# Kernel tuning notes

Hardware: AMD Instinct MI355X
Metric: run time of the kernel (lower is better)

The kernel has to match this reference:

```python
import jax, jax.numpy as jnp
import numpy as np

B, S, D, H = 256, 128, 2, 512


def _lstm_cell(x, h, c, Wih, Whh, bih, bhh):
    # PyTorch LSTMCell gate order: i, f, g, o
    z = x @ Wih.T + bih + h @ Whh.T + bhh
    i, f, g, o = jnp.split(z, 4, axis=-1)
    c_new = jax.nn.sigmoid(f) * c + jax.nn.sigmoid(i) * jnp.tanh(g)
    h_new = jax.nn.sigmoid(o) * jnp.tanh(c_new)
    return h_new, c_new


def setup_inputs() -> dict:
    key = jax.random.key(0)
    ks = jax.random.split(key, 16)
    sc = 0.05
    inp = {
        "x": jax.random.uniform(ks[0], (B, S, D), dtype=jnp.float32),
        "enc_Wih": jax.random.normal(ks[1], (4 * H, D), dtype=jnp.float32) * sc,
        "enc_Whh": jax.random.normal(ks[2], (4 * H, H), dtype=jnp.float32) * sc,
        "enc_bih": jax.random.normal(ks[3], (4 * H,), dtype=jnp.float32) * sc,
        "enc_bhh": jax.random.normal(ks[4], (4 * H,), dtype=jnp.float32) * sc,
        "dec_Wih": jax.random.normal(ks[5], (4 * H, H), dtype=jnp.float32) * sc,
        "dec_Whh": jax.random.normal(ks[6], (4 * H, H), dtype=jnp.float32) * sc,
        "dec_bih": jax.random.normal(ks[7], (4 * H,), dtype=jnp.float32) * sc,
        "dec_bhh": jax.random.normal(ks[8], (4 * H,), dtype=jnp.float32) * sc,
        "W1": jax.random.normal(ks[9], (H, H), dtype=jnp.float32) * sc,
        "b1": jax.random.normal(ks[10], (H,), dtype=jnp.float32) * sc,
        "W2": jax.random.normal(ks[11], (H, H), dtype=jnp.float32) * sc,
        "b2": jax.random.normal(ks[12], (H,), dtype=jnp.float32) * sc,
        "v": jax.random.normal(ks[13], (1, H), dtype=jnp.float32) * sc,
        "bv": jax.random.normal(ks[14], (1,), dtype=jnp.float32) * sc,
    }
    return inp


def reference(x, enc_Wih, enc_Whh, enc_bih, enc_bhh,
              dec_Wih, dec_Whh, dec_bih, dec_bhh,
              W1, b1, W2, b2, v, bv):
    # ---- encoder: LSTMCell scan over sequence ----
    def enc_step(carry, xt):
        h, c = carry
        h, c = _lstm_cell(xt, h, c, enc_Wih, enc_Whh, enc_bih, enc_bhh)
        return (h, c), h

    h0 = jnp.zeros((B, H), dtype=x.dtype)
    c0 = jnp.zeros((B, H), dtype=x.dtype)
    (h_enc, c_enc), enc_hs = jax.lax.scan(enc_step, (h0, c0),
                                          jnp.transpose(x, (1, 0, 2)))
    enc_hs = jnp.transpose(enc_hs, (1, 0, 2))          # [B, S, H]
    W1e = enc_hs @ W1.T + b1                            # [B, S, H]

    # ---- decoder with per-step additive attention ----
    dec_in = jnp.full((B, H), -1.0, dtype=x.dtype)      # constant decoder input

    def dec_step(carry, _):
        h, c = carry
        h, c = _lstm_cell(dec_in, h, c, dec_Wih, dec_Whh, dec_bih, dec_bhh)
        W2h = h @ W2.T + b2                             # [B, H]
        u = jnp.tanh(W1e + W2h[:, None, :]) @ v[0] + bv[0]  # [B, S]
        a = jax.nn.softmax(u, axis=1)                   # [B, S]
        h_new = jnp.einsum('bs,bsh->bh', a, enc_hs)     # attention glimpse
        return (h_new, c), a

    _, attn = jax.lax.scan(dec_step, (h_enc, c_enc), None, length=S)
    return jnp.transpose(attn, (1, 0, 2))               # [B, S, S]
```

## Files before the change

### kernel.cpp

```cpp
#include <hip/hip_runtime.h>

#define B_ 256
#define S_ 128
#define D_ 2
#define H_ 512
#define G4 2048

__device__ __forceinline__ float sigm(float x){ return 1.f/(1.f+__expf(-x)); }
__device__ __forceinline__ float tanh_(float x){ return 1.f - 2.f/(__expf(2.f*x)+1.f); }

__global__ __launch_bounds__(256) void prep_kernel(
    const float* __restrict__ dWih, const float* __restrict__ dbih,
    const float* __restrict__ dbhh, const float* __restrict__ ebih,
    const float* __restrict__ ebhh, float* __restrict__ dxw,
    float* __restrict__ ebias)
{
    int j = blockIdx.x * 256 + threadIdx.x;
    const float* row = dWih + (size_t)j * H_;
    float s = 0.f;
    for (int k = 0; k < H_; k++) s += row[k];
    dxw[j]   = dbih[j] + dbhh[j] - s;
    ebias[j] = ebih[j] + ebhh[j];
}

template<bool ENC>
__global__ __launch_bounds__(256) void lstm_step(
    const float* __restrict__ h_in, int h_stride,
    const float* __restrict__ c_in,
    const float* __restrict__ Whh,
    const float* __restrict__ xbias,
    const float* __restrict__ Wih,
    const float* __restrict__ xt,
    float* __restrict__ h_out, int ho_stride,
    float* __restrict__ c_out)
{
    __shared__ float Hs[32][34];
    __shared__ float Ws[32][68];

    const int tid = threadIdx.x;
    const int tx  = tid & 15;
    const int ty  = tid >> 4;
    const int b0  = blockIdx.x * 32;
    const int kh0 = blockIdx.y * 16;

    float acc[4][2];
#pragma unroll
    for (int g = 0; g < 4; g++) { acc[g][0] = 0.f; acc[g][1] = 0.f; }

    const int lk = tid & 31;
    const int lr = tid >> 5;

    float hreg[4], wreg[8];
#pragma unroll
    for (int i = 0; i < 4; i++) {
        int bl = lr + i * 8;
        hreg[i] = h_in[(size_t)(b0 + bl) * h_stride + lk];
    }
#pragma unroll
    for (int i = 0; i < 8; i++) {
        int p = lr + i * 8; int g = p & 3, kh = p >> 2;
        wreg[i] = Whh[(size_t)(g * H_ + kh0 + kh) * H_ + lk];
    }

    for (int c = 0; c < 16; c++) {
        __syncthreads();
#pragma unroll
        for (int i = 0; i < 4; i++) Hs[lk][lr + i * 8] = hreg[i];
#pragma unroll
        for (int i = 0; i < 8; i++) { int p = lr + i * 8; Ws[lk][p] = wreg[i]; }
        __syncthreads();
        if (c + 1 < 16) {
            int k0 = (c + 1) * 32;
#pragma unroll
            for (int i = 0; i < 4; i++) {
                int bl = lr + i * 8;
                hreg[i] = h_in[(size_t)(b0 + bl) * h_stride + k0 + lk];
            }
#pragma unroll
            for (int i = 0; i < 8; i++) {
                int p = lr + i * 8; int g = p & 3, kh = p >> 2;
                wreg[i] = Whh[(size_t)(g * H_ + kh0 + kh) * H_ + k0 + lk];
            }
        }
#pragma unroll
        for (int k = 0; k < 32; k++) {
            float2 hv = *(const float2*)&Hs[k][2 * ty];
            float4 wv = *(const float4*)&Ws[k][4 * tx];
            acc[0][0] += wv.x * hv.x;  acc[0][1] += wv.x * hv.y;
            acc[1][0] += wv.y * hv.x;  acc[1][1] += wv.y * hv.y;
            acc[2][0] += wv.z * hv.x;  acc[2][1] += wv.z * hv.y;
            acc[3][0] += wv.w * hv.x;  acc[3][1] += wv.w * hv.y;
        }
    }

    const int khid = kh0 + tx;
#pragma unroll
    for (int bb = 0; bb < 2; bb++) {
        int b = b0 + 2 * ty + bb;
        float zi = acc[0][bb] + xbias[0 * H_ + khid];
        float zf = acc[1][bb] + xbias[1 * H_ + khid];
        float zg = acc[2][bb] + xbias[2 * H_ + khid];
        float zo = acc[3][bb] + xbias[3 * H_ + khid];
        if constexpr (ENC) {
            float x0 = xt[b * (S_ * D_) + 0];
            float x1 = xt[b * (S_ * D_) + 1];
            zi += x0 * Wih[(0 * H_ + khid) * D_ + 0] + x1 * Wih[(0 * H_ + khid) * D_ + 1];
            zf += x0 * Wih[(1 * H_ + khid) * D_ + 0] + x1 * Wih[(1 * H_ + khid) * D_ + 1];
            zg += x0 * Wih[(2 * H_ + khid) * D_ + 0] + x1 * Wih[(2 * H_ + khid) * D_ + 1];
            zo += x0 * Wih[(3 * H_ + khid) * D_ + 0] + x1 * Wih[(3 * H_ + khid) * D_ + 1];
        }
        float c_old = c_in[(size_t)b * H_ + khid];
        float ig = sigm(zi), fg = sigm(zf), og = sigm(zo);
        float gg = tanh_(zg);
        float cn = fg * c_old + ig * gg;
        float hn = og * tanh_(cn);
        c_out[(size_t)b * H_ + khid] = cn;
        h_out[(size_t)b * ho_stride + khid] = hn;
    }
}

template<int BM, int BN, int TM, int TN>
__global__ __launch_bounds__((BM/TM)*(BN/TN)) void gemm_bias(
    const float* __restrict__ A, const float* __restrict__ Bm,
    const float* __restrict__ bias, float* __restrict__ C,
    int M, int N, int K)
{
    constexpr int BK = 32;
    constexpr int TH = (BM / TM) * (BN / TN);
    constexpr int AL = BM * BK / TH;
    constexpr int BL = BN * BK / TH;
    constexpr int RP = TH / BK;
    __shared__ float As[BK][BM + 4];
    __shared__ float Bs[BK][BN + 4];
    const int tid = threadIdx.x;
    const int tn = tid % (BN / TN);
    const int tm = tid / (BN / TN);
    const int m0 = blockIdx.x * BM, n0 = blockIdx.y * BN;
    const int lk = tid % BK, lr = tid / BK;

    float acc[TM][TN];
#pragma unroll
    for (int i = 0; i < TM; i++)
#pragma unroll
        for (int j = 0; j < TN; j++) acc[i][j] = 0.f;

    float areg[AL], breg[BL];
#pragma unroll
    for (int i = 0; i < AL; i++) areg[i] = A[(size_t)(m0 + lr + i * RP) * K + lk];
#pragma unroll
    for (int i = 0; i < BL; i++) breg[i] = Bm[(size_t)(n0 + lr + i * RP) * K + lk];

    const int NC = K / BK;
    for (int c = 0; c < NC; c++) {
        __syncthreads();
#pragma unroll
        for (int i = 0; i < AL; i++) As[lk][lr + i * RP] = areg[i];
#pragma unroll
        for (int i = 0; i < BL; i++) Bs[lk][lr + i * RP] = breg[i];
        __syncthreads();
        if (c + 1 < NC) {
            int k0 = (c + 1) * BK;
#pragma unroll
            for (int i = 0; i < AL; i++) areg[i] = A[(size_t)(m0 + lr + i * RP) * K + k0 + lk];
#pragma unroll
            for (int i = 0; i < BL; i++) breg[i] = Bm[(size_t)(n0 + lr + i * RP) * K + k0 + lk];
        }
#pragma unroll
        for (int k = 0; k < BK; k++) {
            float av[TM], bvv[TN];
#pragma unroll
            for (int i = 0; i < TM; i++) av[i] = As[k][tm * TM + i];
#pragma unroll
            for (int j = 0; j < TN; j++) bvv[j] = Bs[k][tn * TN + j];
#pragma unroll
            for (int i = 0; i < TM; i++)
#pragma unroll
                for (int j = 0; j < TN; j++) acc[i][j] += av[i] * bvv[j];
        }
    }
#pragma unroll
    for (int i = 0; i < TM; i++) {
        int m = m0 + tm * TM + i;
#pragma unroll
        for (int j = 0; j < TN; j++) {
            int n = n0 + tn * TN + j;
            C[(size_t)m * N + n] = acc[i][j] + bias[n];
        }
    }
}

__global__ __launch_bounds__(512) void attn_step(
    const float* __restrict__ W1e, const float* __restrict__ enc_hs,
    const float* __restrict__ W2h, const float* __restrict__ vv,
    const float* __restrict__ bv, float* __restrict__ out,
    float* __restrict__ h_glim, int t)
{
    __shared__ float q[H_];
    __shared__ float vs[H_];
    __shared__ float u[S_];
    __shared__ float red[8];

    const int b = blockIdx.x;
    const int tid = threadIdx.x;
    const int lane = tid & 63, wave = tid >> 6;

    q[tid]  = W2h[(size_t)b * H_ + tid];
    vs[tid] = vv[tid];
    __syncthreads();

    const float* w1b = W1e + (size_t)b * S_ * H_;
#pragma unroll 2
    for (int si = 0; si < 16; si++) {
        int s = wave * 16 + si;
        const float* row = w1b + (size_t)s * H_ + lane * 8;
        float4 r0 = *(const float4*)(row);
        float4 r1 = *(const float4*)(row + 4);
        float4 q0 = *(const float4*)&q[lane * 8];
        float4 q1 = *(const float4*)&q[lane * 8 + 4];
        float4 v0 = *(const float4*)&vs[lane * 8];
        float4 v1 = *(const float4*)&vs[lane * 8 + 4];
        float sum = tanh_(r0.x + q0.x) * v0.x + tanh_(r0.y + q0.y) * v0.y
                  + tanh_(r0.z + q0.z) * v0.z + tanh_(r0.w + q0.w) * v0.w
                  + tanh_(r1.x + q1.x) * v1.x + tanh_(r1.y + q1.y) * v1.y
                  + tanh_(r1.z + q1.z) * v1.z + tanh_(r1.w + q1.w) * v1.w;
#pragma unroll
        for (int off = 32; off; off >>= 1) sum += __shfl_xor(sum, off);
        if (lane == 0) u[s] = sum + bv[0];
    }
    __syncthreads();

    float e = 0.f;
    if (tid < 128) {
        float m = u[tid];
#pragma unroll
        for (int off = 32; off; off >>= 1) m = fmaxf(m, __shfl_xor(m, off));
        if ((tid & 63) == 0) red[tid >> 6] = m;
    }
    __syncthreads();
    float mx = fmaxf(red[0], red[1]);
    if (tid < 128) {
        e = __expf(u[tid] - mx);
        float ss = e;
#pragma unroll
        for (int off = 32; off; off >>= 1) ss += __shfl_xor(ss, off);
        if ((tid & 63) == 0) red[4 + (tid >> 6)] = ss;
    }
    __syncthreads();
    float denom = red[4] + red[5];
    if (tid < 128) {
        float a = e / denom;
        u[tid] = a;
        out[(size_t)b * S_ * S_ + (size_t)t * S_ + tid] = a;
    }
    __syncthreads();

    const float* eb = enc_hs + (size_t)b * S_ * H_;
    float acc = 0.f;
#pragma unroll 4
    for (int s = 0; s < S_; s++) acc += u[s] * eb[(size_t)s * H_ + tid];
    h_glim[(size_t)b * H_ + tid] = acc;
}

extern "C" void kernel_launch(void* const* d_in, const int* in_sizes, int n_in,
                              void* d_out, int out_size, void* d_ws, size_t ws_size,
                              hipStream_t stream)
{
    const float* x    = (const float*)d_in[0];
    const float* eWih = (const float*)d_in[1];
    const float* eWhh = (const float*)d_in[2];
    const float* ebih = (const float*)d_in[3];
    const float* ebhh = (const float*)d_in[4];
    const float* dWih = (const float*)d_in[5];
    const float* dWhh = (const float*)d_in[6];
    const float* dbih = (const float*)d_in[7];
    const float* dbhh = (const float*)d_in[8];
    const float* W1   = (const float*)d_in[9];
    const float* b1   = (const float*)d_in[10];
    const float* W2   = (const float*)d_in[11];
    const float* b2   = (const float*)d_in[12];
    const float* vv   = (const float*)d_in[13];
    const float* bv   = (const float*)d_in[14];
    float* out = (float*)d_out;

    float* ws      = (float*)d_ws;
    float* enc_hs  = ws;
    float* W1e     = enc_hs + (size_t)B_ * S_ * H_;
    float* h0      = W1e    + (size_t)B_ * S_ * H_;
    float* c_cur   = h0     + (size_t)B_ * H_;
    float* h_dec   = c_cur  + (size_t)B_ * H_;
    float* h_glim  = h_dec  + (size_t)B_ * H_;
    float* W2h     = h_glim + (size_t)B_ * H_;
    float* dxw     = W2h    + (size_t)B_ * H_;
    float* ebias   = dxw    + G4;

    hipMemsetAsync(h0, 0, (size_t)B_ * H_ * sizeof(float), stream);
    hipMemsetAsync(c_cur, 0, (size_t)B_ * H_ * sizeof(float), stream);
    prep_kernel<<<8, 256, 0, stream>>>(dWih, dbih, dbhh, ebih, ebhh, dxw, ebias);

    dim3 lgrid(B_ / 32, H_ / 16);

    for (int t = 0; t < S_; t++) {
        const float* h_in = (t == 0) ? h0 : (enc_hs + (size_t)(t - 1) * H_);
        int h_stride = (t == 0) ? H_ : S_ * H_;
        lstm_step<true><<<lgrid, 256, 0, stream>>>(
            h_in, h_stride, c_cur, eWhh, ebias, eWih, x + t * D_,
            enc_hs + (size_t)t * H_, S_ * H_, c_cur);
    }

    gemm_bias<64, 64, 4, 4><<<dim3((B_ * S_) / 64, H_ / 64), 256, 0, stream>>>(
        enc_hs, W1, b1, W1e, B_ * S_, H_, H_);

    for (int t = 0; t < S_; t++) {
        const float* h_in = (t == 0) ? (enc_hs + (size_t)(S_ - 1) * H_) : h_glim;
        int h_stride = (t == 0) ? S_ * H_ : H_;
        lstm_step<false><<<lgrid, 256, 0, stream>>>(
            h_in, h_stride, c_cur, dWhh, dxw, nullptr, nullptr,
            h_dec, H_, c_cur);
        gemm_bias<16, 32, 1, 2><<<dim3(B_ / 16, H_ / 32), 256, 0, stream>>>(
            h_dec, W2, b2, W2h, B_, H_, H_);
        attn_step<<<B_, 512, 0, stream>>>(W1e, enc_hs, W2h, vv, bv, out, h_glim, t);
    }
}
```

Measured before the change: 10.52 ms.

## Replace per-step kernel launches with persistent encoder/decoder kernels using grid barriers

Fuses the 128 encoder step launches and the 384 decoder launches into two persistent kernels of 256 blocks that synchronise through an atomic grid barrier. Each thread keeps its slice of the recurrent weight matrix (and of W2) in registers for the whole sequence, and the cell state stays in registers, so weights are not reloaded every step and launch overhead disappears. The risks are a hang if all 256 blocks are not co-resident, since nothing checks occupancy, plus the cost of grid-wide barrier latency and high register pressure from the 64-float weight arrays.

```diff
diff --git a/kernel.cpp b/kernel.cpp
--- a/kernel.cpp
+++ b/kernel.cpp
@@ -4,10 +4,29 @@
 #define S_ 128
 #define D_ 2
 #define H_ 512
-#define G4 2048
+#define NB 256
+#define NT 512
 
 __device__ __forceinline__ float sigm(float x){ return 1.f/(1.f+__expf(-x)); }
 __device__ __forceinline__ float tanh_(float x){ return 1.f - 2.f/(__expf(2.f*x)+1.f); }
+
+__device__ __forceinline__ void grid_barrier(unsigned* bar) {
+    __syncthreads();
+    if (threadIdx.x == 0) {
+        __threadfence();
+        unsigned g = __hip_atomic_load(&bar[1], __ATOMIC_RELAXED, __HIP_MEMORY_SCOPE_AGENT);
+        unsigned a = __hip_atomic_fetch_add(&bar[0], 1u, __ATOMIC_ACQ_REL, __HIP_MEMORY_SCOPE_AGENT);
+        if (a == NB - 1u) {
+            __hip_atomic_store(&bar[0], 0u, __ATOMIC_RELAXED, __HIP_MEMORY_SCOPE_AGENT);
+            __hip_atomic_store(&bar[1], g + 1u, __ATOMIC_RELEASE, __HIP_MEMORY_SCOPE_AGENT);
+        } else {
+            while (__hip_atomic_load(&bar[1], __ATOMIC_RELAXED, __HIP_MEMORY_SCOPE_AGENT) == g)
+                __builtin_amdgcn_s_sleep(2);
+            __threadfence();
+        }
+    }
+    __syncthreads();
+}
 
 __global__ __launch_bounds__(256) void prep_kernel(
     const float* __restrict__ dWih, const float* __restrict__ dbih,
@@ -23,99 +42,102 @@
     ebias[j] = ebih[j] + ebhh[j];
 }
 
-template<bool ENC>
-__global__ __launch_bounds__(256) void lstm_step(
-    const float* __restrict__ h_in, int h_stride,
-    const float* __restrict__ c_in,
-    const float* __restrict__ Whh,
-    const float* __restrict__ xbias,
-    const float* __restrict__ Wih,
-    const float* __restrict__ xt,
-    float* __restrict__ h_out, int ho_stride,
-    float* __restrict__ c_out)
+__global__ __launch_bounds__(NT, 2) void enc_kernel(
+    const float* __restrict__ x, const float* __restrict__ eWih,
+    const float* __restrict__ eWhh, const float* __restrict__ ebias,
+    float* enc_hs, float* c_fin, unsigned* bar)
 {
-    __shared__ float Hs[32][34];
-    __shared__ float Ws[32][68];
+    extern __shared__ float smem[];
+    float (*Hs)[H_]    = (float (*)[H_])smem;
+    float (*Pl)[8][64] = (float (*)[8][64])(smem + 16*H_);
 
     const int tid = threadIdx.x;
-    const int tx  = tid & 15;
-    const int ty  = tid >> 4;
-    const int b0  = blockIdx.x * 32;
-    const int kh0 = blockIdx.y * 16;
-
-    float acc[4][2];
-#pragma unroll
-    for (int g = 0; g < 4; g++) { acc[g][0] = 0.f; acc[g][1] = 0.f; }
-
-    const int lk = tid & 31;
-    const int lr = tid >> 5;
-
-    float hreg[4], wreg[8];
-#pragma unroll
-    for (int i = 0; i < 4; i++) {
-        int bl = lr + i * 8;
-        hreg[i] = h_in[(size_t)(b0 + bl) * h_stride + lk];
-    }
-#pragma unroll
-    for (int i = 0; i < 8; i++) {
-        int p = lr + i * 8; int g = p & 3, kh = p >> 2;
-        wreg[i] = Whh[(size_t)(g * H_ + kh0 + kh) * H_ + lk];
-    }
-
-    for (int c = 0; c < 16; c++) {
-        __syncthreads();
-#pragma unroll
-        for (int i = 0; i < 4; i++) Hs[lk][lr + i * 8] = hreg[i];
-#pragma unroll
-        for (int i = 0; i < 8; i++) { int p = lr + i * 8; Ws[lk][p] = wreg[i]; }
-        __syncthreads();
-        if (c + 1 < 16) {
-            int k0 = (c + 1) * 32;
-#pragma unroll
-            for (int i = 0; i < 4; i++) {
-                int bl = lr + i * 8;
-                hreg[i] = h_in[(size_t)(b0 + bl) * h_stride + k0 + lk];
-            }
-#pragma unroll
-            for (int i = 0; i < 8; i++) {
-                int p = lr + i * 8; int g = p & 3, kh = p >> 2;
-                wreg[i] = Whh[(size_t)(g * H_ + kh0 + kh) * H_ + k0 + lk];
-            }
-        }
-#pragma unroll
-        for (int k = 0; k < 32; k++) {
-            float2 hv = *(const float2*)&Hs[k][2 * ty];
-            float4 wv = *(const float4*)&Ws[k][4 * tx];
-            acc[0][0] += wv.x * hv.x;  acc[0][1] += wv.x * hv.y;
-            acc[1][0] += wv.y * hv.x;  acc[1][1] += wv.y * hv.y;
-            acc[2][0] += wv.z * hv.x;  acc[2][1] += wv.z * hv.y;
-            acc[3][0] += wv.w * hv.x;  acc[3][1] += wv.w * hv.y;
-        }
-    }
-
-    const int khid = kh0 + tx;
-#pragma unroll
-    for (int bb = 0; bb < 2; bb++) {
-        int b = b0 + 2 * ty + bb;
-        float zi = acc[0][bb] + xbias[0 * H_ + khid];
-        float zf = acc[1][bb] + xbias[1 * H_ + khid];
-        float zg = acc[2][bb] + xbias[2 * H_ + khid];
-        float zo = acc[3][bb] + xbias[3 * H_ + khid];
-        if constexpr (ENC) {
-            float x0 = xt[b * (S_ * D_) + 0];
-            float x1 = xt[b * (S_ * D_) + 1];
-            zi += x0 * Wih[(0 * H_ + khid) * D_ + 0] + x1 * Wih[(0 * H_ + khid) * D_ + 1];
-            zf += x0 * Wih[(1 * H_ + khid) * D_ + 0] + x1 * Wih[(1 * H_ + khid) * D_ + 1];
-            zg += x0 * Wih[(2 * H_ + khid) * D_ + 0] + x1 * Wih[(2 * H_ + khid) * D_ + 1];
-            zo += x0 * Wih[(3 * H_ + khid) * D_ + 0] + x1 * Wih[(3 * H_ + khid) * D_ + 1];
-        }
-        float c_old = c_in[(size_t)b * H_ + khid];
-        float ig = sigm(zi), fg = sigm(zf), og = sigm(zo);
-        float gg = tanh_(zg);
-        float cn = fg * c_old + ig * gg;
-        float hn = og * tanh_(cn);
-        c_out[(size_t)b * H_ + khid] = cn;
-        h_out[(size_t)b * ho_stride + khid] = hn;
+    const int wv = tid >> 6, ln = tid & 63;
+    const int bt = blockIdx.x >> 5, jt = blockIdx.x & 31;
+    const int b0 = bt * 32, hu0 = jt * 16;
+    const int lg = ln >> 4, lhu = ln & 15;
+    const int wrow = lg * H_ + hu0 + lhu;
+
+    float w[64];
+    {
+        const float4* wp = (const float4*)(eWhh + (size_t)wrow * H_ + wv * 64);
+#pragma unroll
+        for (int i = 0; i < 16; i++) {
+            float4 t4 = wp[i];
+            w[4*i+0]=t4.x; w[4*i+1]=t4.y; w[4*i+2]=t4.z; w[4*i+3]=t4.w;
+        }
+    }
+    const int fb = tid >> 4, fh = tid & 15;
+    const int fhu = hu0 + fh;
+    float eb4[4] = {0,0,0,0}, wi0[4] = {0,0,0,0}, wi1[4] = {0,0,0,0};
+    if (tid < 256) {
+#pragma unroll
+        for (int g = 0; g < 4; g++) {
+            eb4[g] = ebias[g*H_ + fhu];
+            wi0[g] = eWih[(size_t)(g*H_ + fhu)*D_ + 0];
+            wi1[g] = eWih[(size_t)(g*H_ + fhu)*D_ + 1];
+        }
+    }
+    float creg0 = 0.f, creg1 = 0.f;
+
+    for (int t = 0; t < S_; t++) {
+        const float* hsrc = enc_hs + (size_t)(t-1) * H_;
+#pragma unroll 1
+        for (int bc = 0; bc < 2; bc++) {
+            __syncthreads();
+            {
+                int r = tid >> 5, c0 = (tid & 31) * 4;
+                int b = b0 + bc*16 + r;
+#pragma unroll
+                for (int i = 0; i < 4; i++) {
+                    float4 v4;
+                    if (t == 0) v4 = make_float4(0.f,0.f,0.f,0.f);
+                    else v4 = *(const float4*)(hsrc + (size_t)b * (S_*H_) + c0 + i*128);
+                    *(float4*)&Hs[r][c0 + i*128] = v4;
+                }
+            }
+            __syncthreads();
+#pragma unroll 2
+            for (int b8 = 0; b8 < 16; b8++) {
+                const float4* hp = (const float4*)&Hs[b8][wv * 64];
+                float acc = 0.f;
+#pragma unroll
+                for (int i = 0; i < 16; i++) {
+                    float4 h4 = hp[i];
+                    acc += h4.x*w[4*i] + h4.y*w[4*i+1] + h4.z*w[4*i+2] + h4.w*w[4*i+3];
+                }
+                Pl[b8][wv][ln ^ ((b8 & 15) << 2)] = acc;
+            }
+            __syncthreads();
+            if (tid < 256) {
+                float z4[4];
+#pragma unroll
+                for (int g = 0; g < 4; g++) {
+                    float s = 0.f;
+#pragma unroll
+                    for (int w8 = 0; w8 < 8; w8++)
+                        s += Pl[fb][w8][(g*16 + fh) ^ ((fb & 15) << 2)];
+                    z4[g] = s + eb4[g];
+                }
+                int b = b0 + bc*16 + fb;
+                float x0 = x[(size_t)(b*S_ + t)*D_ + 0];
+                float x1 = x[(size_t)(b*S_ + t)*D_ + 1];
+                float zi = z4[0] + x0*wi0[0] + x1*wi1[0];
+                float zf = z4[1] + x0*wi0[1] + x1*wi1[1];
+                float zg = z4[2] + x0*wi0[2] + x1*wi1[2];
+                float zo = z4[3] + x0*wi0[3] + x1*wi1[3];
+                float cold = bc ? creg1 : creg0;
+                float cn = sigm(zf)*cold + sigm(zi)*tanh_(zg);
+                float hn = sigm(zo)*tanh_(cn);
+                if (bc) creg1 = cn; else creg0 = cn;
+                enc_hs[((size_t)b*S_ + t)*H_ + fhu] = hn;
+            }
+        }
+        if (t < S_-1) grid_barrier(bar);
+    }
+    if (tid < 256) {
+        c_fin[(size_t)(b0 + fb)*H_ + fhu]      = creg0;
+        c_fin[(size_t)(b0 + 16 + fb)*H_ + fhu] = creg1;
     }
 }
 
@@ -189,76 +211,195 @@
     }
 }
 
-__global__ __launch_bounds__(512) void attn_step(
-    const float* __restrict__ W1e, const float* __restrict__ enc_hs,
-    const float* __restrict__ W2h, const float* __restrict__ vv,
-    const float* __restrict__ bv, float* __restrict__ out,
-    float* __restrict__ h_glim, int t)
+__global__ __launch_bounds__(NT, 2) void dec_kernel(
+    const float* __restrict__ dWhh, const float* __restrict__ dxw,
+    const float* __restrict__ W2, const float* __restrict__ b2,
+    const float* __restrict__ vv, const float* __restrict__ bv,
+    const float* __restrict__ enc_hs, const float* __restrict__ W1e,
+    const float* __restrict__ c_fin,
+    float* h_dec, float* W2h, float* h_glim, float* out, unsigned* bar)
 {
-    __shared__ float q[H_];
-    __shared__ float vs[H_];
-    __shared__ float u[S_];
-    __shared__ float red[8];
-
-    const int b = blockIdx.x;
+    extern __shared__ float smem[];
+    float (*Hs)[H_]    = (float (*)[H_])smem;
+    float (*Pl)[8][64] = (float (*)[8][64])(smem + 16*H_);
+    float (*P2)[8][17] = (float (*)[8][17])(smem + 16*H_);
+    float* u   = smem;
+    float* red = smem + 128;
+
     const int tid = threadIdx.x;
-    const int lane = tid & 63, wave = tid >> 6;
-
-    q[tid]  = W2h[(size_t)b * H_ + tid];
-    vs[tid] = vv[tid];
-    __syncthreads();
-
-    const float* w1b = W1e + (size_t)b * S_ * H_;
+    const int wv = tid >> 6, ln = tid & 63;
+    const int bt = blockIdx.x >> 5, jt = blockIdx.x & 31;
+    const int b0 = bt * 32, hu0 = jt * 16;
+    const int lg = ln >> 4, lhu = ln & 15;
+    const int wrow = lg * H_ + hu0 + lhu;
+
+    float w[64];
+    {
+        const float4* wp = (const float4*)(dWhh + (size_t)wrow * H_ + wv * 64);
+#pragma unroll
+        for (int i = 0; i < 16; i++) {
+            float4 t4 = wp[i];
+            w[4*i+0]=t4.x; w[4*i+1]=t4.y; w[4*i+2]=t4.z; w[4*i+3]=t4.w;
+        }
+    }
+    const int n_ = hu0 + lhu;
+    const int kg = wv * 4 + lg;
+    float w2r[16];
+    {
+        const float4* p = (const float4*)(W2 + (size_t)n_ * H_ + kg * 16);
+#pragma unroll
+        for (int i = 0; i < 4; i++) {
+            float4 t4 = p[i];
+            w2r[4*i+0]=t4.x; w2r[4*i+1]=t4.y; w2r[4*i+2]=t4.z; w2r[4*i+3]=t4.w;
+        }
+    }
+    const float4 vr0 = *(const float4*)(vv + ln*8);
+    const float4 vr1 = *(const float4*)(vv + ln*8 + 4);
+    const float bvr = bv[0];
+
+    const int fb = tid >> 4, fh = tid & 15;
+    const int fhu = hu0 + fh;
+    float db4[4] = {0,0,0,0}, b2f = 0.f;
+    float creg0 = 0.f, creg1 = 0.f;
+    if (tid < 256) {
+#pragma unroll
+        for (int g = 0; g < 4; g++) db4[g] = dxw[g*H_ + fhu];
+        b2f = b2[fhu];
+        creg0 = c_fin[(size_t)(b0 + fb)*H_ + fhu];
+        creg1 = c_fin[(size_t)(b0 + 16 + fb)*H_ + fhu];
+    }
+
+    const int bA = blockIdx.x;
+    const float* w1b = W1e + (size_t)bA * S_ * H_;
+    const float* ebA = enc_hs + (size_t)bA * S_ * H_;
+
+    for (int t = 0; t < S_; t++) {
+        const float* hsrc = (t == 0) ? (enc_hs + (size_t)(S_-1)*H_) : h_glim;
+        const size_t hstr = (t == 0) ? (size_t)(S_*H_) : (size_t)H_;
+#pragma unroll 1
+        for (int bc = 0; bc < 2; bc++) {
+            __syncthreads();
+            {
+                int r = tid >> 5, c0 = (tid & 31) * 4;
+                int b = b0 + bc*16 + r;
+#pragma unroll
+                for (int i = 0; i < 4; i++)
+                    *(float4*)&Hs[r][c0 + i*128] =
+                        *(const float4*)(hsrc + (size_t)b * hstr + c0 + i*128);
+            }
+            __syncthreads();
 #pragma unroll 2
-    for (int si = 0; si < 16; si++) {
-        int s = wave * 16 + si;
-        const float* row = w1b + (size_t)s * H_ + lane * 8;
-        float4 r0 = *(const float4*)(row);
-        float4 r1 = *(const float4*)(row + 4);
-        float4 q0 = *(const float4*)&q[lane * 8];
-        float4 q1 = *(const float4*)&q[lane * 8 + 4];
-        float4 v0 = *(const float4*)&vs[lane * 8];
-        float4 v1 = *(const float4*)&vs[lane * 8 + 4];
-        float sum = tanh_(r0.x + q0.x) * v0.x + tanh_(r0.y + q0.y) * v0.y
-                  + tanh_(r0.z + q0.z) * v0.z + tanh_(r0.w + q0.w) * v0.w
-                  + tanh_(r1.x + q1.x) * v1.x + tanh_(r1.y + q1.y) * v1.y
-                  + tanh_(r1.z + q1.z) * v1.z + tanh_(r1.w + q1.w) * v1.w;
-#pragma unroll
-        for (int off = 32; off; off >>= 1) sum += __shfl_xor(sum, off);
-        if (lane == 0) u[s] = sum + bv[0];
-    }
-    __syncthreads();
-
-    float e = 0.f;
-    if (tid < 128) {
-        float m = u[tid];
-#pragma unroll
-        for (int off = 32; off; off >>= 1) m = fmaxf(m, __shfl_xor(m, off));
-        if ((tid & 63) == 0) red[tid >> 6] = m;
-    }
-    __syncthreads();
-    float mx = fmaxf(red[0], red[1]);
-    if (tid < 128) {
-        e = __expf(u[tid] - mx);
-        float ss = e;
-#pragma unroll
-        for (int off = 32; off; off >>= 1) ss += __shfl_xor(ss, off);
-        if ((tid & 63) == 0) red[4 + (tid >> 6)] = ss;
-    }
-    __syncthreads();
-    float denom = red[4] + red[5];
-    if (tid < 128) {
-        float a = e / denom;
-        u[tid] = a;
-        out[(size_t)b * S_ * S_ + (size_t)t * S_ + tid] = a;
-    }
-    __syncthreads();
-
-    const float* eb = enc_hs + (size_t)b * S_ * H_;
-    float acc = 0.f;
+            for (int b8 = 0; b8 < 16; b8++) {
+                const float4* hp = (const float4*)&Hs[b8][wv * 64];
+                float acc = 0.f;
+#pragma unroll
+                for (int i = 0; i < 16; i++) {
+                    float4 h4 = hp[i];
+                    acc += h4.x*w[4*i] + h4.y*w[4*i+1] + h4.z*w[4*i+2] + h4.w*w[4*i+3];
+                }
+                Pl[b8][wv][ln ^ ((b8 & 15) << 2)] = acc;
+            }
+            __syncthreads();
+            if (tid < 256) {
+                float z4[4];
+#pragma unroll
+                for (int g = 0; g < 4; g++) {
+                    float s = 0.f;
+#pragma unroll
+                    for (int w8 = 0; w8 < 8; w8++)
+                        s += Pl[fb][w8][(g*16 + fh) ^ ((fb & 15) << 2)];
+                    z4[g] = s + db4[g];
+                }
+                int b = b0 + bc*16 + fb;
+                float cold = bc ? creg1 : creg0;
+                float cn = sigm(z4[1])*cold + sigm(z4[0])*tanh_(z4[2]);
+                float hn = sigm(z4[3])*tanh_(cn);
+                if (bc) creg1 = cn; else creg0 = cn;
+                h_dec[(size_t)b*H_ + fhu] = hn;
+            }
+        }
+        grid_barrier(bar);
+#pragma unroll 1
+        for (int bc = 0; bc < 2; bc++) {
+            __syncthreads();
+            {
+                int r = tid >> 5, c0 = (tid & 31) * 4;
+                int b = b0 + bc*16 + r;
+#pragma unroll
+                for (int i = 0; i < 4; i++)
+                    *(float4*)&Hs[r][c0 + i*128] =
+                        *(const float4*)(h_dec + (size_t)b * H_ + c0 + i*128);
+            }
+            __syncthreads();
+#pragma unroll 2
+            for (int b8 = 0; b8 < 16; b8++) {
+                const float4* hp = (const float4*)&Hs[b8][kg * 16];
+                float p = 0.f;
+#pragma unroll
+                for (int i = 0; i < 4; i++) {
+                    float4 h4 = hp[i];
+                    p += h4.x*w2r[4*i] + h4.y*w2r[4*i+1] + h4.z*w2r[4*i+2] + h4.w*w2r[4*i+3];
+                }
+                p += __shfl_xor(p, 16);
+                p += __shfl_xor(p, 32);
+                if (lg == 0) P2[b8][wv][lhu] = p;
+            }
+            __syncthreads();
+            if (tid < 256) {
+                float s = 0.f;
+#pragma unroll
+                for (int w8 = 0; w8 < 8; w8++) s += P2[fb][w8][fh];
+                W2h[(size_t)(b0 + bc*16 + fb)*H_ + hu0 + fh] = s + b2f;
+            }
+        }
+        grid_barrier(bar);
+        {
+            float4 q0 = *(const float4*)(W2h + (size_t)bA*H_ + ln*8);
+            float4 q1 = *(const float4*)(W2h + (size_t)bA*H_ + ln*8 + 4);
+#pragma unroll 2
+            for (int si = 0; si < 16; si++) {
+                int s = wv*16 + si;
+                const float4* rp = (const float4*)(w1b + (size_t)s*H_ + ln*8);
+                float4 r0 = rp[0], r1 = rp[1];
+                float sum = tanh_(r0.x+q0.x)*vr0.x + tanh_(r0.y+q0.y)*vr0.y
+                          + tanh_(r0.z+q0.z)*vr0.z + tanh_(r0.w+q0.w)*vr0.w
+                          + tanh_(r1.x+q1.x)*vr1.x + tanh_(r1.y+q1.y)*vr1.y
+                          + tanh_(r1.z+q1.z)*vr1.z + tanh_(r1.w+q1.w)*vr1.w;
+#pragma unroll
+                for (int off = 32; off; off >>= 1) sum += __shfl_xor(sum, off);
+                if (ln == 0) u[s] = sum + bvr;
+            }
+            __syncthreads();
+            float e = 0.f;
+            if (tid < 128) {
+                float m = u[tid];
+#pragma unroll
+                for (int off = 32; off; off >>= 1) m = fmaxf(m, __shfl_xor(m, off));
+                if (ln == 0) red[tid >> 6] = m;
+            }
+            __syncthreads();
+            if (tid < 128) {
+                float mx = fmaxf(red[0], red[1]);
+                e = __expf(u[tid] - mx);
+                float ss = e;
+#pragma unroll
+                for (int off = 32; off; off >>= 1) ss += __shfl_xor(ss, off);
+                if (ln == 0) red[2 + (tid >> 6)] = ss;
+            }
+            __syncthreads();
+            if (tid < 128) {
+                float a = e / (red[2] + red[3]);
+                u[tid] = a;
+                out[(size_t)bA*S_*S_ + (size_t)t*S_ + tid] = a;
+            }
+            __syncthreads();
+            float acc = 0.f;
 #pragma unroll 4
-    for (int s = 0; s < S_; s++) acc += u[s] * eb[(size_t)s * H_ + tid];
-    h_glim[(size_t)b * H_ + tid] = acc;
+            for (int s = 0; s < S_; s++) acc += u[s] * ebA[(size_t)s*H_ + tid];
+            h_glim[(size_t)bA*H_ + tid] = acc;
+        }
+        if (t < S_-1) grid_barrier(bar);
+    }
 }
 
 extern "C" void kernel_launch(void* const* d_in, const int* in_sizes, int n_in,
@@ -285,39 +426,23 @@
     float* ws      = (float*)d_ws;
     float* enc_hs  = ws;
     float* W1e     = enc_hs + (size_t)B_ * S_ * H_;
-    float* h0      = W1e    + (size_t)B_ * S_ * H_;
-    float* c_cur   = h0     + (size_t)B_ * H_;
-    float* h_dec   = c_cur  + (size_t)B_ * H_;
-    float* h_glim  = h_dec  + (size_t)B_ * H_;
-    float* W2h     = h_glim + (size_t)B_ * H_;
-    float* dxw     = W2h    + (size_t)B_ * H_;
-    float* ebias   = dxw    + G4;
-
-    hipMemsetAsync(h0, 0, (size_t)B_ * H_ * sizeof(float), stream);
-    hipMemsetAsync(c_cur, 0, (size_t)B_ * H_ * sizeof(float), stream);
+    float* h_dec   = W1e    + (size_t)B_ * S_ * H_;
+    float* W2h     = h_dec  + (size_t)B_ * H_;
+    float* h_glim  = W2h    + (size_t)B_ * H_;
+    float* c_fin   = h_glim + (size_t)B_ * H_;
+    float* dxw     = c_fin  + (size_t)B_ * H_;
+    float* ebias   = dxw    + 2048;
+    unsigned* bar  = (unsigned*)(ebias + 2048);
+
+    hipMemsetAsync(bar, 0, 2 * sizeof(unsigned), stream);
     prep_kernel<<<8, 256, 0, stream>>>(dWih, dbih, dbhh, ebih, ebhh, dxw, ebias);
 
-    dim3 lgrid(B_ / 32, H_ / 16);
-
-    for (int t = 0; t < S_; t++) {
-        const float* h_in = (t == 0) ? h0 : (enc_hs + (size_t)(t - 1) * H_);
-        int h_stride = (t == 0) ? H_ : S_ * H_;
-        lstm_step<true><<<lgrid, 256, 0, stream>>>(
-            h_in, h_stride, c_cur, eWhh, ebias, eWih, x + t * D_,
-            enc_hs + (size_t)t * H_, S_ * H_, c_cur);
-    }
-
-    gemm_bias<64, 64, 4, 4><<<dim3((B_ * S_) / 64, H_ / 64), 256, 0, stream>>>(
-        enc_hs, W1, b1, W1e, B_ * S_, H_, H_);
-
-    for (int t = 0; t < S_; t++) {
-        const float* h_in = (t == 0) ? (enc_hs + (size_t)(S_ - 1) * H_) : h_glim;
-        int h_stride = (t == 0) ? S_ * H_ : H_;
-        lstm_step<false><<<lgrid, 256, 0, stream>>>(
-            h_in, h_stride, c_cur, dWhh, dxw, nullptr, nullptr,
-            h_dec, H_, c_cur);
-        gemm_bias<16, 32, 1, 2><<<dim3(B_ / 16, H_ / 32), 256, 0, stream>>>(
-            h_dec, W2, b2, W2h, B_, H_, H_);
-        attn_step<<<B_, 512, 0, stream>>>(W1e, enc_hs, W2h, vv, bv, out, h_glim, t);
-    }
-}
+    enc_kernel<<<NB, NT, 64*1024, stream>>>(x, eWih, eWhh, ebias, enc_hs, c_fin, bar);
+
+    gemm_bias<64, 64, 4, 4><<<dim3((B_*S_)/64, H_/64), 256, 0, stream>>>(
+        enc_hs, W1, b1, W1e, B_*S_, H_, H_);
+
+    dec_kernel<<<NB, NT, 64*1024, stream>>>(dWhh, dxw, W2, b2, vv, bv,
+                                            enc_hs, W1e, c_fin,
+                                            h_dec, W2h, h_glim, out, bar);
+}
```

Measured after the change: 21.63 ms. +105.6%, slower.

## Register-resident split-K LSTM step, pre-packed Whh, fuse W2 projection into attention

Applied to the files above, without the earlier changes.

Rewrites the per-step LSTM kernel to hold a 64-wide K-slice of Whh in registers per thread and reduce partial sums across 8 K-slices through shared memory. A one-time pack kernel reorders Whh for coalesced float4 loads, with a fallback to the unpacked layout when the workspace is too small. The decoder's separate W2h GEMM launch is removed by computing h_dec·W2^T (from a pre-transposed W2) inside the attention kernel. The changes aim to cut launch count and weight-load inefficiency per timestep. In exchange the code carries heavy register pressure (64 weights plus 16 accumulators per thread) and redundant W2 reads in every attention block.

```diff
diff --git a/kernel.cpp b/kernel.cpp
--- a/kernel.cpp
+++ b/kernel.cpp
@@ -4,118 +4,124 @@
 #define S_ 128
 #define D_ 2
 #define H_ 512
-#define G4 2048
 
 __device__ __forceinline__ float sigm(float x){ return 1.f/(1.f+__expf(-x)); }
 __device__ __forceinline__ float tanh_(float x){ return 1.f - 2.f/(__expf(2.f*x)+1.f); }
 
-__global__ __launch_bounds__(256) void prep_kernel(
+__global__ __launch_bounds__(256) void prep3(
     const float* __restrict__ dWih, const float* __restrict__ dbih,
     const float* __restrict__ dbhh, const float* __restrict__ ebih,
-    const float* __restrict__ ebhh, float* __restrict__ dxw,
-    float* __restrict__ ebias)
-{
-    int j = blockIdx.x * 256 + threadIdx.x;
-    const float* row = dWih + (size_t)j * H_;
-    float s = 0.f;
-    for (int k = 0; k < H_; k++) s += row[k];
-    dxw[j]   = dbih[j] + dbhh[j] - s;
-    ebias[j] = ebih[j] + ebhh[j];
+    const float* __restrict__ ebhh, const float* __restrict__ W2,
+    float* __restrict__ dxw, float* __restrict__ ebias, float* __restrict__ W2T)
+{
+    int bx = blockIdx.x, tid = threadIdx.x;
+    if (bx < 8) {
+        int j = bx * 256 + tid;
+        const float* row = dWih + (size_t)j * H_;
+        float s = 0.f;
+        for (int k = 0; k < H_; k++) s += row[k];
+        dxw[j]   = dbih[j] + dbhh[j] - s;
+        ebias[j] = ebih[j] + ebhh[j];
+    } else {
+        int i = (bx - 8) * 256 + tid;
+        int k = i >> 9, j = i & 511;
+        W2T[(size_t)k * H_ + j] = W2[(size_t)j * H_ + k];
+    }
+}
+
+__global__ __launch_bounds__(256) void pack_whh(
+    const float* __restrict__ eW, const float* __restrict__ dW,
+    float* __restrict__ pe, float* __restrict__ pd)
+{
+    size_t n = (size_t)blockIdx.x * 256 + threadIdx.x;
+    int sel = (int)(n >> 20);
+    int m = (int)(n & 1048575);
+    int c = m & 3, rw = (m >> 2) & 63, i4 = (m >> 8) & 15;
+    int ks = (m >> 12) & 7, jt = m >> 15;
+    int g = rw >> 4, hu = rw & 15;
+    size_t src = (size_t)(g * H_ + jt * 16 + hu) * H_ + ks * 64 + i4 * 4 + c;
+    if (sel) pd[m] = dW[src]; else pe[m] = eW[src];
 }
 
 template<bool ENC>
-__global__ __launch_bounds__(256) void lstm_step(
-    const float* __restrict__ h_in, int h_stride,
-    const float* __restrict__ c_in,
-    const float* __restrict__ Whh,
+__global__ __launch_bounds__(512) void lstm_step3(
+    const float* __restrict__ Wsrc, int packed,
+    const float* __restrict__ h_in, long hstr, int hzero,
+    float* __restrict__ c_st, int czero,
     const float* __restrict__ xbias,
-    const float* __restrict__ Wih,
-    const float* __restrict__ xt,
-    float* __restrict__ h_out, int ho_stride,
-    float* __restrict__ c_out)
-{
-    __shared__ float Hs[32][34];
-    __shared__ float Ws[32][68];
-
+    const float* __restrict__ Wih, const float* __restrict__ xt,
+    float* __restrict__ h_out, long hostr)
+{
+    __shared__ float P[8][64][20];
     const int tid = threadIdx.x;
-    const int tx  = tid & 15;
-    const int ty  = tid >> 4;
-    const int b0  = blockIdx.x * 32;
-    const int kh0 = blockIdx.y * 16;
-
-    float acc[4][2];
-#pragma unroll
-    for (int g = 0; g < 4; g++) { acc[g][0] = 0.f; acc[g][1] = 0.f; }
-
-    const int lk = tid & 31;
-    const int lr = tid >> 5;
-
-    float hreg[4], wreg[8];
-#pragma unroll
-    for (int i = 0; i < 4; i++) {
-        int bl = lr + i * 8;
-        hreg[i] = h_in[(size_t)(b0 + bl) * h_stride + lk];
-    }
-#pragma unroll
-    for (int i = 0; i < 8; i++) {
-        int p = lr + i * 8; int g = p & 3, kh = p >> 2;
-        wreg[i] = Whh[(size_t)(g * H_ + kh0 + kh) * H_ + lk];
-    }
-
-    for (int c = 0; c < 16; c++) {
-        __syncthreads();
-#pragma unroll
-        for (int i = 0; i < 4; i++) Hs[lk][lr + i * 8] = hreg[i];
-#pragma unroll
-        for (int i = 0; i < 8; i++) { int p = lr + i * 8; Ws[lk][p] = wreg[i]; }
-        __syncthreads();
-        if (c + 1 < 16) {
-            int k0 = (c + 1) * 32;
-#pragma unroll
-            for (int i = 0; i < 4; i++) {
-                int bl = lr + i * 8;
-                hreg[i] = h_in[(size_t)(b0 + bl) * h_stride + k0 + lk];
-            }
-#pragma unroll
-            for (int i = 0; i < 8; i++) {
-                int p = lr + i * 8; int g = p & 3, kh = p >> 2;
-                wreg[i] = Whh[(size_t)(g * H_ + kh0 + kh) * H_ + k0 + lk];
-            }
-        }
-#pragma unroll
-        for (int k = 0; k < 32; k++) {
-            float2 hv = *(const float2*)&Hs[k][2 * ty];
-            float4 wv = *(const float4*)&Ws[k][4 * tx];
-            acc[0][0] += wv.x * hv.x;  acc[0][1] += wv.x * hv.y;
-            acc[1][0] += wv.y * hv.x;  acc[1][1] += wv.y * hv.y;
-            acc[2][0] += wv.z * hv.x;  acc[2][1] += wv.z * hv.y;
-            acc[3][0] += wv.w * hv.x;  acc[3][1] += wv.w * hv.y;
-        }
-    }
-
-    const int khid = kh0 + tx;
-#pragma unroll
-    for (int bb = 0; bb < 2; bb++) {
-        int b = b0 + 2 * ty + bb;
-        float zi = acc[0][bb] + xbias[0 * H_ + khid];
-        float zf = acc[1][bb] + xbias[1 * H_ + khid];
-        float zg = acc[2][bb] + xbias[2 * H_ + khid];
-        float zo = acc[3][bb] + xbias[3 * H_ + khid];
+    const int rw = tid & 63;
+    const int ks = __builtin_amdgcn_readfirstlane(tid >> 6);
+    const int bx = blockIdx.x;
+    const int bt = bx & 15, jt = bx >> 4;
+    const int b0 = bt * 16;
+    const int g = rw >> 4, hu = rw & 15;
+
+    float w[64];
+    if (packed) {
+        const float4* wp = (const float4*)Wsrc + ((size_t)(jt * 8 + ks) * 16) * 64 + rw;
+#pragma unroll
+        for (int i = 0; i < 16; i++) {
+            float4 t4 = wp[(size_t)i * 64];
+            w[4*i+0]=t4.x; w[4*i+1]=t4.y; w[4*i+2]=t4.z; w[4*i+3]=t4.w;
+        }
+    } else {
+        const float4* wp = (const float4*)(Wsrc + (size_t)(g * H_ + jt * 16 + hu) * H_ + ks * 64);
+#pragma unroll
+        for (int i = 0; i < 16; i++) {
+            float4 t4 = wp[i];
+            w[4*i+0]=t4.x; w[4*i+1]=t4.y; w[4*i+2]=t4.z; w[4*i+3]=t4.w;
+        }
+    }
+
+    float acc[16];
+#pragma unroll
+    for (int b = 0; b < 16; b++) acc[b] = 0.f;
+    if (!hzero) {
+#pragma unroll
+        for (int b = 0; b < 16; b++) {
+            const float* hb = h_in + (size_t)(b0 + b) * hstr + ks * 64;
+            float s = 0.f;
+#pragma unroll
+            for (int i = 0; i < 64; i++) s += hb[i] * w[i];
+            acc[b] = s;
+        }
+    }
+#pragma unroll
+    for (int b4 = 0; b4 < 4; b4++)
+        *(float4*)&P[ks][rw][b4 * 4] =
+            make_float4(acc[b4*4], acc[b4*4+1], acc[b4*4+2], acc[b4*4+3]);
+    __syncthreads();
+
+    if (tid < 256) {
+        int b = tid & 15, h2 = tid >> 4;
+        float z[4];
+#pragma unroll
+        for (int gg = 0; gg < 4; gg++) {
+            int row = gg * 16 + h2;
+            float s = 0.f;
+#pragma unroll
+            for (int k8 = 0; k8 < 8; k8++) s += P[k8][row][b];
+            z[gg] = s + xbias[gg * H_ + jt * 16 + h2];
+        }
+        int bb = b0 + b, hj = jt * 16 + h2;
         if constexpr (ENC) {
-            float x0 = xt[b * (S_ * D_) + 0];
-            float x1 = xt[b * (S_ * D_) + 1];
-            zi += x0 * Wih[(0 * H_ + khid) * D_ + 0] + x1 * Wih[(0 * H_ + khid) * D_ + 1];
-            zf += x0 * Wih[(1 * H_ + khid) * D_ + 0] + x1 * Wih[(1 * H_ + khid) * D_ + 1];
-            zg += x0 * Wih[(2 * H_ + khid) * D_ + 0] + x1 * Wih[(2 * H_ + khid) * D_ + 1];
-            zo += x0 * Wih[(3 * H_ + khid) * D_ + 0] + x1 * Wih[(3 * H_ + khid) * D_ + 1];
-        }
-        float c_old = c_in[(size_t)b * H_ + khid];
-        float ig = sigm(zi), fg = sigm(zf), og = sigm(zo);
-        float gg = tanh_(zg);
-        float cn = fg * c_old + ig * gg;
-        float hn = og * tanh_(cn);
-        c_out[(size_t)b * H_ + khid] = cn;
-        h_out[(size_t)b * ho_stride + khid] = hn;
+            float x0 = xt[(size_t)bb * (S_ * D_) + 0];
+            float x1 = xt[(size_t)bb * (S_ * D_) + 1];
+#pragma unroll
+            for (int gg = 0; gg < 4; gg++)
+                z[gg] += x0 * Wih[(size_t)(gg * H_ + hj) * D_ + 0]
+                       + x1 * Wih[(size_t)(gg * H_ + hj) * D_ + 1];
+        }
+        float cold = czero ? 0.f : c_st[(size_t)bb * H_ + hj];
+        float cn = sigm(z[1]) * cold + sigm(z[0]) * tanh_(z[2]);
+        float hn = sigm(z[3]) * tanh_(cn);
+        c_st[(size_t)bb * H_ + hj] = cn;
+        h_out[(size_t)bb * hostr + hj] = hn;
     }
 }
 
@@ -189,76 +195,92 @@
     }
 }
 
-__global__ __launch_bounds__(512) void attn_step(
-    const float* __restrict__ W1e, const float* __restrict__ enc_hs,
-    const float* __restrict__ W2h, const float* __restrict__ vv,
-    const float* __restrict__ bv, float* __restrict__ out,
+__global__ __launch_bounds__(512) void attn_fused(
+    const float* __restrict__ W2T, const float* __restrict__ b2,
+    const float* __restrict__ vv, const float* __restrict__ bv,
+    const float* __restrict__ h_dec, const float* __restrict__ W1e,
+    const float* __restrict__ enc_hs, float* __restrict__ out,
     float* __restrict__ h_glim, int t)
 {
-    __shared__ float q[H_];
-    __shared__ float vs[H_];
-    __shared__ float u[S_];
+    __shared__ float hs[H_];
+    __shared__ float qq[H_];
+    __shared__ float pw[4][H_];
+    __shared__ float ua[S_];
     __shared__ float red[8];
-
+    const int tid = threadIdx.x;
     const int b = blockIdx.x;
-    const int tid = threadIdx.x;
-    const int lane = tid & 63, wave = tid >> 6;
-
-    q[tid]  = W2h[(size_t)b * H_ + tid];
-    vs[tid] = vv[tid];
-    __syncthreads();
-
+    const int ln = tid & 63, wv = tid >> 6;
+
+    if (tid < 128)
+        *(float4*)&hs[tid * 4] = *(const float4*)&h_dec[(size_t)b * H_ + tid * 4];
+    __syncthreads();
+
+    {
+        const int j4 = tid & 127, kh = tid >> 7;
+        float4 a4 = make_float4(0.f, 0.f, 0.f, 0.f);
+        const float4* wp = (const float4*)W2T + j4;
+        int kbeg = kh * 128;
+#pragma unroll 4
+        for (int k = kbeg; k < kbeg + 128; k++) {
+            float4 w4 = wp[(size_t)k * 128];
+            float hk = hs[k];
+            a4.x += w4.x * hk; a4.y += w4.y * hk;
+            a4.z += w4.z * hk; a4.w += w4.w * hk;
+        }
+        *(float4*)&pw[kh][j4 * 4] = a4;
+    }
+    __syncthreads();
+    qq[tid] = pw[0][tid] + pw[1][tid] + pw[2][tid] + pw[3][tid] + b2[tid];
+    __syncthreads();
+
+    float4 q0 = *(float4*)&qq[ln * 8], q1 = *(float4*)&qq[ln * 8 + 4];
+    float4 v0 = *(const float4*)(vv + ln * 8), v1 = *(const float4*)(vv + ln * 8 + 4);
+    const float bvr = bv[0];
     const float* w1b = W1e + (size_t)b * S_ * H_;
 #pragma unroll 2
     for (int si = 0; si < 16; si++) {
-        int s = wave * 16 + si;
-        const float* row = w1b + (size_t)s * H_ + lane * 8;
-        float4 r0 = *(const float4*)(row);
-        float4 r1 = *(const float4*)(row + 4);
-        float4 q0 = *(const float4*)&q[lane * 8];
-        float4 q1 = *(const float4*)&q[lane * 8 + 4];
-        float4 v0 = *(const float4*)&vs[lane * 8];
-        float4 v1 = *(const float4*)&vs[lane * 8 + 4];
+        int s = wv * 16 + si;
+        const float4* rp = (const float4*)(w1b + (size_t)s * H_ + ln * 8);
+        float4 r0 = rp[0], r1 = rp[1];
         float sum = tanh_(r0.x + q0.x) * v0.x + tanh_(r0.y + q0.y) * v0.y
                   + tanh_(r0.z + q0.z) * v0.z + tanh_(r0.w + q0.w) * v0.w
                   + tanh_(r1.x + q1.x) * v1.x + tanh_(r1.y + q1.y) * v1.y
                   + tanh_(r1.z + q1.z) * v1.z + tanh_(r1.w + q1.w) * v1.w;
 #pragma unroll
         for (int off = 32; off; off >>= 1) sum += __shfl_xor(sum, off);
-        if (lane == 0) u[s] = sum + bv[0];
+        if (ln == 0) ua[s] = sum + bvr;
     }
     __syncthreads();
 
     float e = 0.f;
     if (tid < 128) {
-        float m = u[tid];
+        float m = ua[tid];
 #pragma unroll
         for (int off = 32; off; off >>= 1) m = fmaxf(m, __shfl_xor(m, off));
-        if ((tid & 63) == 0) red[tid >> 6] = m;
-    }
-    __syncthreads();
-    float mx = fmaxf(red[0], red[1]);
+        if (ln == 0) red[tid >> 6] = m;
+    }
+    __syncthreads();
     if (tid < 128) {
-        e = __expf(u[tid] - mx);
+        float mx = fmaxf(red[0], red[1]);
+        e = __expf(ua[tid] - mx);
         float ss = e;
 #pragma unroll
         for (int off = 32; off; off >>= 1) ss += __shfl_xor(ss, off);
-        if ((tid & 63) == 0) red[4 + (tid >> 6)] = ss;
-    }
-    __syncthreads();
-    float denom = red[4] + red[5];
+        if (ln == 0) red[2 + (tid >> 6)] = ss;
+    }
+    __syncthreads();
     if (tid < 128) {
-        float a = e / denom;
-        u[tid] = a;
+        float a = e / (red[2] + red[3]);
+        ua[tid] = a;
         out[(size_t)b * S_ * S_ + (size_t)t * S_ + tid] = a;
     }
     __syncthreads();
 
     const float* eb = enc_hs + (size_t)b * S_ * H_;
-    float acc = 0.f;
+    float ga = 0.f;
 #pragma unroll 4
-    for (int s = 0; s < S_; s++) acc += u[s] * eb[(size_t)s * H_ + tid];
-    h_glim[(size_t)b * H_ + tid] = acc;
+    for (int s = 0; s < S_; s++) ga += ua[s] * eb[(size_t)s * H_ + tid];
+    h_glim[(size_t)b * H_ + tid] = ga;
 }
 
 extern "C" void kernel_launch(void* const* d_in, const int* in_sizes, int n_in,
@@ -282,29 +304,36 @@
     const float* bv   = (const float*)d_in[14];
     float* out = (float*)d_out;
 
-    float* ws      = (float*)d_ws;
-    float* enc_hs  = ws;
-    float* W1e     = enc_hs + (size_t)B_ * S_ * H_;
-    float* h0      = W1e    + (size_t)B_ * S_ * H_;
-    float* c_cur   = h0     + (size_t)B_ * H_;
-    float* h_dec   = c_cur  + (size_t)B_ * H_;
-    float* h_glim  = h_dec  + (size_t)B_ * H_;
-    float* W2h     = h_glim + (size_t)B_ * H_;
-    float* dxw     = W2h    + (size_t)B_ * H_;
-    float* ebias   = dxw    + G4;
-
-    hipMemsetAsync(h0, 0, (size_t)B_ * H_ * sizeof(float), stream);
-    hipMemsetAsync(c_cur, 0, (size_t)B_ * H_ * sizeof(float), stream);
-    prep_kernel<<<8, 256, 0, stream>>>(dWih, dbih, dbhh, ebih, ebhh, dxw, ebias);
-
-    dim3 lgrid(B_ / 32, H_ / 16);
+    float* ws     = (float*)d_ws;
+    float* enc_hs = ws;
+    float* W1e    = enc_hs + (size_t)B_ * S_ * H_;
+    float* h_dec  = W1e    + (size_t)B_ * S_ * H_;
+    float* h_glim = h_dec  + (size_t)B_ * H_;
+    float* c_cur  = h_glim + (size_t)B_ * H_;
+    float* W2T    = c_cur  + (size_t)B_ * H_;
+    float* dxw    = W2T    + (size_t)H_ * H_;
+    float* ebias  = dxw    + 2048;
+    float* wpk_e  = ebias  + 2048;
+    float* wpk_d  = wpk_e  + 1048576;
+
+    size_t base_f = (size_t)(wpk_e - ws);
+    int packed = (ws_size >= (base_f + 2u * 1048576u) * sizeof(float)) ? 1 : 0;
+
+    prep3<<<1032, 256, 0, stream>>>(dWih, dbih, dbhh, ebih, ebhh, W2,
+                                    dxw, ebias, W2T);
+    if (packed)
+        pack_whh<<<8192, 256, 0, stream>>>(eWhh, dWhh, wpk_e, wpk_d);
+
+    const float* We = packed ? wpk_e : eWhh;
+    const float* Wd = packed ? wpk_d : dWhh;
 
     for (int t = 0; t < S_; t++) {
-        const float* h_in = (t == 0) ? h0 : (enc_hs + (size_t)(t - 1) * H_);
-        int h_stride = (t == 0) ? H_ : S_ * H_;
-        lstm_step<true><<<lgrid, 256, 0, stream>>>(
-            h_in, h_stride, c_cur, eWhh, ebias, eWih, x + t * D_,
-            enc_hs + (size_t)t * H_, S_ * H_, c_cur);
+        lstm_step3<true><<<512, 512, 0, stream>>>(
+            We, packed,
+            enc_hs + (size_t)(t - 1) * H_, (long)(S_ * H_), (t == 0) ? 1 : 0,
+            c_cur, (t == 0) ? 1 : 0,
+            ebias, eWih, x + (size_t)t * D_,
+            enc_hs + (size_t)t * H_, (long)(S_ * H_));
     }
 
     gemm_bias<64, 64, 4, 4><<<dim3((B_ * S_) / 64, H_ / 64), 256, 0, stream>>>(
@@ -312,12 +341,12 @@
 
     for (int t = 0; t < S_; t++) {
         const float* h_in = (t == 0) ? (enc_hs + (size_t)(S_ - 1) * H_) : h_glim;
-        int h_stride = (t == 0) ? S_ * H_ : H_;
-        lstm_step<false><<<lgrid, 256, 0, stream>>>(
-            h_in, h_stride, c_cur, dWhh, dxw, nullptr, nullptr,
-            h_dec, H_, c_cur);
-        gemm_bias<16, 32, 1, 2><<<dim3(B_ / 16, H_ / 32), 256, 0, stream>>>(
-            h_dec, W2, b2, W2h, B_, H_, H_);
-        attn_step<<<B_, 512, 0, stream>>>(W1e, enc_hs, W2h, vv, bv, out, h_glim, t);
-    }
-}
+        long hstr = (t == 0) ? (long)(S_ * H_) : (long)H_;
+        lstm_step3<false><<<512, 512, 0, stream>>>(
+            Wd, packed, h_in, hstr, 0,
+            c_cur, 0, dxw, nullptr, nullptr,
+            h_dec, (long)H_);
+        attn_fused<<<B_, 512, 0, stream>>>(W2T, b2, vv, bv,
+                                           h_dec, W1e, enc_hs, out, h_glim, t);
+    }
+}
```

After: 13.35 ms. 1.27x slower.
